# Optimization experiments

Measured on AMD Instinct MI355X. Metric: run time of the kernel, lower is better.

The kernel has to match this reference:

```python
import jax, jax.numpy as jnp
import numpy as np

B, S, D = 16, 1024, 1024
H = 8
QK = D // 8            # qk_dim = dim / qk_dim_div(8) = 128
EXP = D * 2            # expand_dim = dim * expand_factor(2) = 2048
V = D                  # v_dim = dim
RESIDUAL_DEPTH = 384   # hyp['net']['residual_depth'] (init scale only)
NUM_BLOCKS = 8         # hyp['net']['num_blocks'] (init scale only)
NEG = -1e30            # stand-in for -inf in the masked positions


def setup_inputs() -> dict:
    key = jax.random.key(0)
    k0, k1, k2 = jax.random.split(key, 3)
    x = jax.random.normal(k0, (B, S, D), jnp.float32)
    norm_w = jnp.ones((D,), jnp.float32)  # LayerNorm weight (bias=False)
    expand_w = (0.5 / RESIDUAL_DEPTH**0.5 / 2.0) * jax.random.normal(
        k1, (2 * QK + 2 * EXP, D), jnp.float32)
    project_w = (1.0 / RESIDUAL_DEPTH**0.5 / 2.0 / NUM_BLOCKS) * jax.random.normal(
        k2, (D, EXP), jnp.float32)
    pos_bias_mult = jnp.array(1.0, jnp.float32)
    return {
        "x": x,
        "norm_w": norm_w,
        "expand_w": expand_w,
        "project_w": project_w,
        "pos_bias_mult": pos_bias_mult,
        "first_acting_token_idx": 512,
        "last_acting_token_idx": 768,
    }


def _make_mask(pos_bias_mult, seq_len, first_idx, last_idx, dtype):
    idx = jnp.arange(seq_len)
    rel = (idx[None, :] - idx[:, None]).astype(dtype)   # j - i  (ALiBi-like)
    causal = idx[None, :] <= idx[:, None]               # tril incl. diagonal
    bias = jax.nn.softplus(pos_bias_mult) * rel
    mask = jnp.where(causal, bias, NEG)
    if first_idx is not None:
        assert last_idx is not None and last_idx > first_idx
        # torch: idx >= seq_len -> None -> slice from 0
        fi = 0 if first_idx >= seq_len else first_idx
        li = 0 if last_idx >= seq_len else last_idx
        override = (idx[:, None] >= fi) & (idx[None, :] >= li)
        mask = jnp.where(override, bias, mask)
    return mask


def reference(x, norm_w, expand_w, project_w, pos_bias_mult,
              first_acting_token_idx, last_acting_token_idx):
    Bx, Sx, Dx = x.shape
    residual = x
    mask = _make_mask(pos_bias_mult, Sx, first_acting_token_idx,
                      last_acting_token_idx, x.dtype)  # [S, S]

    # LayerNorm (bias-free)
    mu = x.mean(-1, keepdims=True)
    xc = x - mu
    var = (xc * xc).mean(-1, keepdims=True)
    xn = xc * jax.lax.rsqrt(var + 1e-5) * norm_w

    # fused expand projection, then split q / k / linear / pre_gelu
    proj = jnp.einsum('bsd,ed->bse', xn, expand_w)
    q = proj[..., :QK]
    k = proj[..., QK:2 * QK]
    lin = proj[..., 2 * QK:2 * QK + EXP]
    pre = proj[..., 2 * QK + EXP:]
    geglu = lin * jax.nn.gelu(pre, approximate=False)

    # linear_value = False: both local and attention-value come from geglu
    geglu_local = geglu[..., :EXP - V]   # [B, S, EXP-V]
    geglu_value = geglu[..., EXP - V:]   # [B, S, V]

    dh_q = QK // H
    dh_v = V // H
    qh = q.reshape(Bx, Sx, H, dh_q).transpose(0, 2, 1, 3)
    kh = k.reshape(Bx, Sx, H, dh_q).transpose(0, 2, 1, 3)
    vh = geglu_value.reshape(Bx, Sx, H, dh_v).transpose(0, 2, 1, 3)

    scale = 1.0 / np.sqrt(dh_q)  # SDPA default: 1/sqrt(E), E = query head dim
    scores = jnp.einsum('bhqd,bhkd->bhqk', qh, kh) * scale + mask
    attn = jax.nn.softmax(scores, axis=-1)
    outh = jnp.einsum('bhqk,bhkd->bhqd', attn, vh)
    attention = outh.transpose(0, 2, 1, 3).reshape(Bx, Sx, V)
    # NOTE: geglu_local's head rearrange + inverse rearrange is an identity.

    out = jnp.einsum('bse,de->bsd',
                     jnp.concatenate([geglu_local, attention], axis=-1),
                     project_w)
    return residual + out
```

## Files before the change

kernel.cpp:

```cpp
#include <hip/hip_runtime.h>
#include <hip/hip_bf16.h>
#include <cstdint>
#include <cstddef>

#define S_LEN   1024
#define D_DIM   1024
#define QK_DIM  128
#define EXP_DIM 2048
#define H_HEADS 8
#define DH_Q    16
#define DH_V    128
#define M_ROWS  16384

typedef __bf16 bf16;
typedef __bf16 b16x4 __attribute__((ext_vector_type(4)));
typedef __bf16 b16x8 __attribute__((ext_vector_type(8)));
typedef float  fx4   __attribute__((ext_vector_type(4)));
typedef float  f32x16 __attribute__((ext_vector_type(16)));

__device__ __forceinline__ void load_lds16(const bf16* g, bf16* l) {
    __builtin_amdgcn_global_load_lds(
        (const __attribute__((address_space(1))) void*)g,
        (__attribute__((address_space(3))) void*)l, 16, 0, 0);
}

__global__ __launch_bounds__(256) void convert_kernel(const float* __restrict__ src,
                                                      bf16* __restrict__ dst, int n4) {
    const int i = blockIdx.x * 256 + threadIdx.x;
    if (i >= n4) return;
    const fx4 v = ((const fx4*)src)[i];
    b16x4 o;
#pragma unroll
    for (int k = 0; k < 4; ++k) o[k] = (bf16)v[k];
    ((b16x4*)dst)[i] = o;
}

__global__ __launch_bounds__(256) void convert_expand_kernel(const float* __restrict__ src,
                                                             bf16* __restrict__ dst) {
    const int i = blockIdx.x * 256 + threadIdx.x;
    const int orow = i >> 8, col = i & 255;
    int irow;
    if (orow < 256) {
        irow = orow;
    } else {
        const int t = orow - 256;
        const int c = t >> 5, j = t & 31;
        irow = (j < 16) ? (256 + c * 16 + j) : (2304 + c * 16 + (j - 16));
    }
    const fx4 v = ((const fx4*)src)[irow * 256 + col];
    b16x4 o;
#pragma unroll
    for (int k = 0; k < 4; ++k) o[k] = (bf16)v[k];
    ((b16x4*)dst)[i] = o;
}

__global__ __launch_bounds__(256) void ln_kernel(const float* __restrict__ x,
                                                 const float* __restrict__ w,
                                                 bf16* __restrict__ xn) {
    const int row = blockIdx.x;
    const int tid = threadIdx.x;
    const fx4 t = ((const fx4*)x)[(size_t)row * 256 + tid];
    float v[4];
    float s = 0.f, ss = 0.f;
#pragma unroll
    for (int i = 0; i < 4; ++i) { v[i] = t[i]; s += v[i]; ss += v[i] * v[i]; }
#pragma unroll
    for (int off = 32; off >= 1; off >>= 1) {
        s  += __shfl_xor(s,  off);
        ss += __shfl_xor(ss, off);
    }
    __shared__ float ls[4], lss[4];
    const int wave = tid >> 6;
    if ((tid & 63) == 0) { ls[wave] = s; lss[wave] = ss; }
    __syncthreads();
    s  = ls[0]  + ls[1]  + ls[2]  + ls[3];
    ss = lss[0] + lss[1] + lss[2] + lss[3];
    const float mu  = s * (1.f / D_DIM);
    const float var = ss * (1.f / D_DIM) - mu * mu;
    const float r   = rsqrtf(var + 1e-5f);
    const fx4 w4 = ((const fx4*)w)[tid];
    b16x4 o4;
#pragma unroll
    for (int i = 0; i < 4; ++i) o4[i] = (bf16)((v[i] - mu) * r * w4[i]);
    ((b16x4*)(xn + (size_t)row * D_DIM))[tid] = o4;
}

__device__ __forceinline__ float gelu_exact(float x) {
    return 0.5f * x * (1.f + erff(x * 0.70710678118654752f));
}

__device__ __forceinline__ void tile_map(int& tm, int& tn) {
    const int NT = gridDim.x, MT = gridDim.y;
    const int lin = blockIdx.y * NT + blockIdx.x;
    if ((MT & 31) == 0 && (NT & 3) == 0) {
        const int xcd = lin & 7, slot = lin >> 3;
        const int MB  = MT >> 3;
        const int cnc = NT >> 2;
        const int c = slot >> 4, w = slot & 15;
        const int cm = c / cnc, cn = c - cm * cnc;
        tm = xcd * MB + cm * 4 + (w >> 2);
        tn = cn * 4 + (w & 3);
    } else { tm = blockIdx.y; tn = blockIdx.x; }
}

__device__ __forceinline__ void tile_map256(int& tm, int& tn) {
    const int NT = gridDim.x, MT = gridDim.y;
    const int lin = blockIdx.y * NT + blockIdx.x;
    if ((MT & 31) == 0 && (NT & 3) == 0) {
        const int xcd = lin & 7, slot = lin >> 3;
        const int MB  = MT >> 3;
        const int cnc = NT >> 2;
        const int c = slot >> 4, w = slot & 15;
        const int cm = c / cnc, cn = c - cm * cnc;
        tm = xcd * MB + cm * 4 + (w >> 2);
        tn = cn * 4 + (w & 3);
    } else { tm = blockIdx.y; tn = blockIdx.x; }
}

template <int EPI>
__global__ __launch_bounds__(256) void gemm_bt(const bf16* __restrict__ A,
                                               const bf16* __restrict__ W,
                                               const float* __restrict__ R,
                                               bf16* __restrict__ C,
                                               bf16* __restrict__ VH,
                                               float* __restrict__ OutF,
                                               int M, int N, int K) {
    __shared__ bf16 As[128 * 32];
    __shared__ bf16 Ws[128 * 32];
    const int tid  = threadIdx.x;
    const int wave = tid >> 6, lane = tid & 63;
    int tmi, tni;
    tile_map(tmi, tni);
    const int tile_n = tni * 128;
    const int tile_m = tmi * 128;
    const int m_off = (wave >> 1) * 64, n_off = (wave & 1) * 64;

    fx4 acc[4][4] = {};

    const int c0 = wave * 128 + lane;
    const int c1 = c0 + 64;
    const int r0 = c0 >> 2, cc0 = (c0 & 3) * 8;
    const int r1 = c1 >> 2, cc1 = (c1 & 3) * 8;

    const int mrow = lane & 15, quad = lane >> 4;

    for (int k0 = 0; k0 < K; k0 += 32) {
        load_lds16(A + (size_t)(tile_m + r0) * K + k0 + cc0, &As[c0 * 8]);
        load_lds16(A + (size_t)(tile_m + r1) * K + k0 + cc1, &As[c1 * 8]);
        load_lds16(W + (size_t)(tile_n + r0) * K + k0 + cc0, &Ws[c0 * 8]);
        load_lds16(W + (size_t)(tile_n + r1) * K + k0 + cc1, &Ws[c1 * 8]);
        __syncthreads();

        b16x8 af[4], bfr[4];
#pragma unroll
        for (int i = 0; i < 4; ++i) {
            af[i]  = *(const b16x8*)&As[(m_off + i * 16 + mrow) * 32 + quad * 8];
            bfr[i] = *(const b16x8*)&Ws[(n_off + i * 16 + mrow) * 32 + quad * 8];
        }
#pragma unroll
        for (int mi = 0; mi < 4; ++mi)
#pragma unroll
            for (int ni = 0; ni < 4; ++ni)
                acc[mi][ni] = __builtin_amdgcn_mfma_f32_16x16x32_bf16(
                    af[mi], bfr[ni], acc[mi][ni], 0, 0, 0);
        __syncthreads();
    }

    const int lcol = lane & 15, lrow4 = (lane >> 4) * 4;
#pragma unroll
    for (int mi = 0; mi < 4; ++mi)
#pragma unroll
        for (int ni = 0; ni < 4; ++ni)
#pragma unroll
            for (int r = 0; r < 4; ++r) {
                const int gr = tile_m + m_off + mi * 16 + lrow4 + r;
                const int gc = tile_n + n_off + ni * 16 + lcol;
                const float a = acc[mi][ni][r];
                if (EPI == 0) {
                    C[(size_t)gr * N + gc] = (bf16)a;
                } else if (EPI == 1) {
                    const size_t idx = (size_t)gr * N + gc;
                    OutF[idx] = a + R[idx];
                }
            }
}

__device__ __forceinline__ b16x8 lds_frag_swz(const bf16* buf, int r, int colb) {
    const int p = (r << 7) + ((((colb >> 4) ^ r) & 7) << 4) + (colb & 15);
    return *(const b16x8*)((const char*)buf + p);
}

template <int EPI>
__global__ __launch_bounds__(512, 2) void gemm256(const bf16* __restrict__ A,
                                                  const bf16* __restrict__ W,
                                                  const float* __restrict__ R,
                                                  bf16* __restrict__ C,
                                                  bf16* __restrict__ VH,
                                                  float* __restrict__ OutF,
                                                  int M, int N, int K) {
    __shared__ bf16 Abuf[2][16384];
    __shared__ bf16 Bbuf[2][16384];
    const int tid  = threadIdx.x;
    const int wave = tid >> 6, lane = tid & 63;
    const int wm = wave >> 2, wn = wave & 3;
    const int l15 = lane & 15, quad = lane >> 4;

    int tmi, tni;
    tile_map256(tmi, tni);
    const int tile_m = tmi * 256, tile_n = tni * 256;

    const int srow = tid >> 3;
    const int scol = (((tid & 7) ^ ((tid >> 3) & 7))) * 8;
    size_t offA[4], offB[4];
#pragma unroll
    for (int s = 0; s < 4; ++s) {
        offA[s] = (size_t)(tile_m + s * 64 + srow) * K + scol;
        offB[s] = (size_t)(tile_n + s * 64 + srow) * K + scol;
    }
    const int ldst = tid * 16;

    fx4 acc[8][4] = {};

    const int ntk = K >> 6;
    {
        char* a0 = (char*)&Abuf[0][0] + ldst;
        char* b0 = (char*)&Bbuf[0][0] + ldst;
        load_lds16(A + offA[0], (bf16*)(a0));
        load_lds16(A + offA[2], (bf16*)(a0 + 16384));
        load_lds16(W + offB[0], (bf16*)(b0));
        load_lds16(W + offB[1], (bf16*)(b0 + 8192));
        load_lds16(W + offB[2], (bf16*)(b0 + 16384));
        load_lds16(W + offB[3], (bf16*)(b0 + 24576));
        load_lds16(A + offA[1], (bf16*)(a0 + 8192));
        load_lds16(A + offA[3], (bf16*)(a0 + 24576));
    }

    for (int t = 0; t < ntk; ++t) {
        const int nb = t & 1;
        const int kt1 = (t + 1) << 6;
        const bool pf = (t + 1 < ntk);
        const bf16* ab = &Abuf[nb][0];
        const bf16* bb = &Bbuf[nb][0];
        char* adst = (char*)&Abuf[nb ^ 1][0] + ldst;
        char* bdst = (char*)&Bbuf[nb ^ 1][0] + ldst;

        b16x8 af[4][2];
        b16x8 bfv[2][2];

        asm volatile("s_waitcnt vmcnt(2)" ::: "memory");
        __builtin_amdgcn_s_barrier();
        __builtin_amdgcn_sched_barrier(0);
#pragma unroll
        for (int mi = 0; mi < 4; ++mi)
#pragma unroll
            for (int kk = 0; kk < 2; ++kk)
                af[mi][kk] = lds_frag_swz(ab, wm * 128 + mi * 16 + l15, kk * 64 + quad * 16);
#pragma unroll
        for (int ni = 0; ni < 2; ++ni)
#pragma unroll
            for (int kk = 0; kk < 2; ++kk)
                bfv[ni][kk] = lds_frag_swz(bb, wn * 64 + ni * 16 + l15, kk * 64 + quad * 16);
        if (pf) {
            load_lds16(A + offA[0] + kt1, (bf16*)(adst));
            load_lds16(A + offA[2] + kt1, (bf16*)(adst + 16384));
        }
        __builtin_amdgcn_s_setprio(1);
#pragma unroll
        for (int mi = 0; mi < 4; ++mi)
#pragma unroll
            for (int ni = 0; ni < 2; ++ni)
#pragma unroll
                for (int kk = 0; kk < 2; ++kk)
                    acc[mi][ni] = __builtin_amdgcn_mfma_f32_16x16x32_bf16(
                        af[mi][kk], bfv[ni][kk], acc[mi][ni], 0, 0, 0);
        __builtin_amdgcn_s_setprio(0);

        __builtin_amdgcn_s_barrier();
        __builtin_amdgcn_sched_barrier(0);
#pragma unroll
        for (int ni = 0; ni < 2; ++ni)
#pragma unroll
            for (int kk = 0; kk < 2; ++kk)
                bfv[ni][kk] = lds_frag_swz(bb, wn * 64 + (ni + 2) * 16 + l15, kk * 64 + quad * 16);
        if (pf) {
            load_lds16(W + offB[0] + kt1, (bf16*)(bdst));
            load_lds16(W + offB[1] + kt1, (bf16*)(bdst + 8192));
            load_lds16(W + offB[2] + kt1, (bf16*)(bdst + 16384));
            load_lds16(W + offB[3] + kt1, (bf16*)(bdst + 24576));
        }
        __builtin_amdgcn_s_setprio(1);
#pragma unroll
        for (int mi = 0; mi < 4; ++mi)
#pragma unroll
            for (int ni = 0; ni < 2; ++ni)
#pragma unroll
                for (int kk = 0; kk < 2; ++kk)
                    acc[mi][ni + 2] = __builtin_amdgcn_mfma_f32_16x16x32_bf16(
                        af[mi][kk], bfv[ni][kk], acc[mi][ni + 2], 0, 0, 0);
        __builtin_amdgcn_s_setprio(0);

        if (pf) asm volatile("s_waitcnt vmcnt(6)" ::: "memory");
        else    asm volatile("s_waitcnt vmcnt(0)" ::: "memory");
        __builtin_amdgcn_s_barrier();
        __builtin_amdgcn_sched_barrier(0);
#pragma unroll
        for (int mi = 0; mi < 4; ++mi)
#pragma unroll
            for (int kk = 0; kk < 2; ++kk)
                af[mi][kk] = lds_frag_swz(ab, wm * 128 + (mi + 4) * 16 + l15, kk * 64 + quad * 16);
        if (pf) {
            load_lds16(A + offA[1] + kt1, (bf16*)(adst + 8192));
            load_lds16(A + offA[3] + kt1, (bf16*)(adst + 24576));
        }
        __builtin_amdgcn_s_setprio(1);
#pragma unroll
        for (int mi = 0; mi < 4; ++mi)
#pragma unroll
            for (int ni = 0; ni < 2; ++ni)
#pragma unroll
                for (int kk = 0; kk < 2; ++kk)
                    acc[mi + 4][ni + 2] = __builtin_amdgcn_mfma_f32_16x16x32_bf16(
                        af[mi][kk], bfv[ni][kk], acc[mi + 4][ni + 2], 0, 0, 0);
        __builtin_amdgcn_s_setprio(0);

        __builtin_amdgcn_s_barrier();
        __builtin_amdgcn_sched_barrier(0);
#pragma unroll
        for (int ni = 0; ni < 2; ++ni)
#pragma unroll
            for (int kk = 0; kk < 2; ++kk)
                bfv[ni][kk] = lds_frag_swz(bb, wn * 64 + ni * 16 + l15, kk * 64 + quad * 16);
        __builtin_amdgcn_s_setprio(1);
#pragma unroll
        for (int mi = 0; mi < 4; ++mi)
#pragma unroll
            for (int ni = 0; ni < 2; ++ni)
#pragma unroll
                for (int kk = 0; kk < 2; ++kk)
                    acc[mi + 4][ni] = __builtin_amdgcn_mfma_f32_16x16x32_bf16(
                        af[mi][kk], bfv[ni][kk], acc[mi + 4][ni], 0, 0, 0);
        __builtin_amdgcn_s_setprio(0);
        __builtin_amdgcn_s_barrier();
        __builtin_amdgcn_sched_barrier(0);
    }

    const int rbase = tile_m + wm * 128 + quad * 4;
    if (EPI == 2) {
        const int gb = ((tile_n + wn * 64) >> 1) + l15;
#pragma unroll
        for (int mi = 0; mi < 8; ++mi)
#pragma unroll
            for (int np = 0; np < 2; ++np) {
                const int gcol = gb + np * 16;
#pragma unroll
                for (int r = 0; r < 4; ++r) {
                    const int gr = rbase + mi * 16 + r;
                    const float l = acc[mi][2 * np][r];
                    const float p = acc[mi][2 * np + 1][r];
                    const float g = l * gelu_exact(p);
                    if (gcol < 1024) C[(size_t)gr * 2048 + gcol] = (bf16)g;
                    else             VH[(size_t)gr * 1024 + (gcol - 1024)] = (bf16)g;
                }
            }
    } else {
#pragma unroll
        for (int mi = 0; mi < 8; ++mi)
#pragma unroll
            for (int ni = 0; ni < 4; ++ni)
#pragma unroll
                for (int r = 0; r < 4; ++r) {
                    const int gr = rbase + mi * 16 + r;
                    const int gc = tile_n + wn * 64 + ni * 16 + l15;
                    const float a = acc[mi][ni][r];
                    if (EPI == 0) {
                        C[(size_t)gr * N + gc] = (bf16)a;
                    } else {
                        const size_t idx = (size_t)gr * N + gc;
                        OutF[idx] = a + R[idx];
                    }
                }
    }
}

__global__ __launch_bounds__(512) void attn_kernel(const bf16* __restrict__ qk,
                                                   const bf16* __restrict__ vh,
                                                   const float* __restrict__ pbmv,
                                                   const int* __restrict__ fip,
                                                   const int* __restrict__ lip,
                                                   bf16* __restrict__ concatb) {
    const int lin = blockIdx.y * gridDim.x + blockIdx.x;
    const int xcd = lin & 7, slot = lin >> 3;
    const int bh = xcd * 16 + (slot >> 3);
    const int qt = slot & 7;
    const int b = bh >> 3, h = bh & 7;
    const int q0 = qt * 128;
    const int tid  = threadIdx.x;
    const int wave = tid >> 6, lane = tid & 63;
    const int lm = lane & 31, lh = lane >> 5;
    const int qq = wave >> 1, sect = wave & 1;

    __shared__ float Ps[128][68];
    __shared__ bf16  Pb[128][72];
    __shared__ bf16  Vt[128][72];
    __shared__ float Mrow[128], Lrow[128], Arow[128];

    const float pm = pbmv[0];
    const float sp = (pm > 20.f) ? pm : log1pf(expf(pm));
    int fi = fip[0], li = lip[0];
    if (fi >= S_LEN) fi = 0;
    if (li >= S_LEN) li = 0;

    const b16x8 qfrag = *(const b16x8*)(qk
        + ((size_t)(b * S_LEN + q0 + qq * 32 + lm)) * 256 + h * DH_Q + lh * 8);

    f32x16 accO[2] = {};
    if (tid < 128) { Mrow[tid] = -3e38f; Lrow[tid] = 0.f; }

    const int vkey = tid & 63;
    const int vd   = (tid >> 6) * 16;
    const int srow = wave * 16 + (lane >> 2);
    const int skq  = (lane & 3) * 16;

    const int qmax = q0 + 127;
    for (int k0 = 0; k0 < S_LEN; k0 += 64) {
        const bool any = (k0 <= qmax) || ((qmax >= fi) && (k0 + 63 >= li));
        if (!any) continue;

        __syncthreads();

#pragma unroll
        for (int i = 0; i < 2; ++i) {
            const int d0 = vd + i * 8;
            const b16x8 v8 = *(const b16x8*)(vh
                + ((size_t)(b * S_LEN + k0 + vkey)) * D_DIM + h * DH_V + d0);
#pragma unroll
            for (int j = 0; j < 8; ++j) Vt[d0 + j][vkey] = v8[j];
        }

        {
            const b16x8 kfrag = *(const b16x8*)(qk
                + ((size_t)(b * S_LEN + k0 + sect * 32 + lm)) * 256
                + QK_DIM + h * DH_Q + lh * 8);
            f32x16 z = {};
            const f32x16 S = __builtin_amdgcn_mfma_f32_32x32x16_bf16(qfrag, kfrag, z, 0, 0, 0);
#pragma unroll
            for (int r = 0; r < 16; ++r) {
                const int row = qq * 32 + (r & 3) + 8 * (r >> 2) + 4 * lh;
                Ps[row][sect * 32 + lm] = S[r];
            }
        }
        __syncthreads();

        {
            const int rg = q0 + srow;
            float s[16];
#pragma unroll
            for (int i = 0; i < 4; ++i) {
                const fx4 t = *(const fx4*)&Ps[srow][skq + i * 4];
#pragma unroll
                for (int j = 0; j < 4; ++j) {
                    const int jg = k0 + skq + i * 4 + j;
                    const bool act = (jg <= rg) || ((rg >= fi) && (jg >= li));
                    s[i * 4 + j] = act ? (t[j] * 0.25f + sp * (float)(jg - rg)) : -3e38f;
                }
            }
            float mloc = -3e38f;
#pragma unroll
            for (int i = 0; i < 16; ++i) mloc = fmaxf(mloc, s[i]);
            mloc = fmaxf(mloc, __shfl_xor(mloc, 1));
            mloc = fmaxf(mloc, __shfl_xor(mloc, 2));
            const float m_old = Mrow[srow];
            const float m_new = fmaxf(m_old, mloc);
            const float alpha = (m_old <= -1e29f) ? 0.f : __expf(m_old - m_new);
            float lsum = 0.f;
            b16x8 p0, p1;
#pragma unroll
            for (int i = 0; i < 16; ++i) {
                const float p = (s[i] <= -1e29f) ? 0.f : __expf(s[i] - m_new);
                lsum += p;
                if (i < 8) p0[i] = (bf16)p; else p1[i - 8] = (bf16)p;
            }
            lsum += __shfl_xor(lsum, 1);
            lsum += __shfl_xor(lsum, 2);
            *(b16x8*)&Pb[srow][skq]     = p0;
            *(b16x8*)&Pb[srow][skq + 8] = p1;
            if ((lane & 3) == 0) {
                Mrow[srow] = m_new;
                Lrow[srow] = alpha * Lrow[srow] + lsum;
                Arow[srow] = alpha;
            }
        }
        __syncthreads();

        {
#pragma unroll
            for (int r = 0; r < 16; ++r) {
                const float al = Arow[qq * 32 + (r & 3) + 8 * (r >> 2) + 4 * lh];
                accO[0][r] *= al;
                accO[1][r] *= al;
            }
            b16x8 Af[4];
#pragma unroll
            for (int ks = 0; ks < 4; ++ks)
                Af[ks] = *(const b16x8*)&Pb[qq * 32 + lm][ks * 16 + lh * 8];
#pragma unroll
            for (int nb = 0; nb < 2; ++nb)
#pragma unroll
                for (int ks = 0; ks < 4; ++ks) {
                    const b16x8 Bf = *(const b16x8*)&Vt[sect * 64 + nb * 32 + lm][ks * 16 + lh * 8];
                    accO[nb] = __builtin_amdgcn_mfma_f32_32x32x16_bf16(Af[ks], Bf, accO[nb], 0, 0, 0);
                }
        }
    }

#pragma unroll
    for (int r = 0; r < 16; ++r) {
        const int row = qq * 32 + (r & 3) + 8 * (r >> 2) + 4 * lh;
        const float L = Lrow[row];
        const float inv = (L > 0.f) ? 1.f / L : 0.f;
        const size_t base = ((size_t)(b * S_LEN + q0 + row)) * EXP_DIM
                          + EXP_DIM / 2 + h * DH_V + sect * 64 + lm;
#pragma unroll
        for (int nb = 0; nb < 2; ++nb)
            concatb[base + nb * 32] = (bf16)(accO[nb][r] * inv);
    }
}

static constexpr size_t WS0_OFF = 0;
static constexpr size_t QK_OFF  = 67108864;
static constexpr size_t VH_OFF  = QK_OFF + 8388608;
static constexpr size_t EW_OFF  = VH_OFF + 33554432;
static constexpr size_t PW_OFF  = EW_OFF + 8912896;
static constexpr size_t WS_NEED = PW_OFF + 4194304;

extern "C" void kernel_launch(void* const* d_in, const int* in_sizes, int n_in,
                              void* d_out, int out_size, void* d_ws, size_t ws_size,
                              hipStream_t stream) {
    const float* x         = (const float*)d_in[0];
    const float* norm_w    = (const float*)d_in[1];
    const float* expand_w  = (const float*)d_in[2];
    const float* project_w = (const float*)d_in[3];
    const float* pbm       = (const float*)d_in[4];
    const int*   fip       = (const int*)d_in[5];
    const int*   lip       = (const int*)d_in[6];
    float* out = (float*)d_out;

    if (ws_size < WS_NEED) return;

    char* ws = (char*)d_ws;
    bf16* ws0 = (bf16*)(ws + WS0_OFF);
    bf16* qkb = (bf16*)(ws + QK_OFF);
    bf16* vh  = (bf16*)(ws + VH_OFF);
    bf16* ewb = (bf16*)(ws + EW_OFF);
    bf16* pwb = (bf16*)(ws + PW_OFF);
    bf16* xn  = (bf16*)d_out;

    convert_expand_kernel<<<4352, 256, 0, stream>>>(expand_w, ewb);
    convert_kernel<<<2048, 256, 0, stream>>>(project_w, pwb, 2097152 / 4);
    ln_kernel<<<M_ROWS, 256, 0, stream>>>(x, norm_w, xn);

    gemm_bt<0><<<dim3(2, M_ROWS / 128), 256, 0, stream>>>(
        xn, ewb, nullptr, qkb, nullptr, nullptr, M_ROWS, 256, D_DIM);
    gemm256<2><<<dim3(16, M_ROWS / 256), 512, 0, stream>>>(
        xn, ewb + (size_t)256 * D_DIM, nullptr, ws0, vh, nullptr, M_ROWS, 4096, D_DIM);
    attn_kernel<<<dim3(64, 16), 512, 0, stream>>>(qkb, vh, pbm, fip, lip, ws0);
    gemm256<1><<<dim3(4, M_ROWS / 256), 512, 0, stream>>>(
        ws0, pwb, x, nullptr, nullptr, out, M_ROWS, D_DIM, EXP_DIM);
}
```

Measured before the change: 505.4 us.

## Keep attention scores in registers via transposed MFMA and per-section row stats

Computes S^T with swapped MFMA operands so each lane holds one query row's scores, applying the mask, scale and bias and running the online softmax in registers instead of staging fp32 scores through LDS. Row max is combined across the two key sections through a small shared buffer, and running max/sum are kept per lane, with sums merged at the end. P fragments are assembled with cross-half shuffles and reused directly as MFMA A operands for the local half, cutting LDS traffic. This adds shuffle work and a small reduction sync, and it changes the softmax work split across lanes.

```diff
diff --git a/kernel.cpp b/kernel.cpp
--- a/kernel.cpp
+++ b/kernel.cpp
@@ -399,10 +399,11 @@
     const int lm = lane & 31, lh = lane >> 5;
     const int qq = wave >> 1, sect = wave & 1;
 
-    __shared__ float Ps[128][68];
     __shared__ bf16  Pb[128][72];
     __shared__ bf16  Vt[128][72];
-    __shared__ float Mrow[128], Lrow[128], Arow[128];
+    __shared__ float Msect[2][128];
+    __shared__ float Lsect[2][128];
+    __shared__ float Arow[128];
 
     const float pm = pbmv[0];
     const float sp = (pm > 20.f) ? pm : log1pf(expf(pm));
@@ -414,12 +415,12 @@
         + ((size_t)(b * S_LEN + q0 + qq * 32 + lm)) * 256 + h * DH_Q + lh * 8);
 
     f32x16 accO[2] = {};
-    if (tid < 128) { Mrow[tid] = -3e38f; Lrow[tid] = 0.f; }
+    float m_run = -3e38f, l_run = 0.f;
 
     const int vkey = tid & 63;
     const int vd   = (tid >> 6) * 16;
-    const int srow = wave * 16 + (lane >> 2);
-    const int skq  = (lane & 3) * 16;
+    const int myrow = qq * 32 + lm;
+    const int rg    = q0 + myrow;
 
     const int qmax = q0 + 127;
     for (int k0 = 0; k0 < S_LEN; k0 += 64) {
@@ -437,58 +438,62 @@
             for (int j = 0; j < 8; ++j) Vt[d0 + j][vkey] = v8[j];
         }
 
+        float s[16];
+        float mx = -3e38f;
         {
             const b16x8 kfrag = *(const b16x8*)(qk
                 + ((size_t)(b * S_LEN + k0 + sect * 32 + lm)) * 256
                 + QK_DIM + h * DH_Q + lh * 8);
             f32x16 z = {};
-            const f32x16 S = __builtin_amdgcn_mfma_f32_32x32x16_bf16(qfrag, kfrag, z, 0, 0, 0);
+            const f32x16 S = __builtin_amdgcn_mfma_f32_32x32x16_bf16(kfrag, qfrag, z, 0, 0, 0);
 #pragma unroll
             for (int r = 0; r < 16; ++r) {
-                const int row = qq * 32 + (r & 3) + 8 * (r >> 2) + 4 * lh;
-                Ps[row][sect * 32 + lm] = S[r];
+                const int jg = k0 + sect * 32 + (r & 3) + 8 * (r >> 2) + 4 * lh;
+                const bool act = (jg <= rg) || ((rg >= fi) && (jg >= li));
+                s[r] = act ? (S[r] * 0.25f + sp * (float)(jg - rg)) : -3e38f;
+                mx = fmaxf(mx, s[r]);
             }
         }
+        mx = fmaxf(mx, __shfl_xor(mx, 32));
+        if (lh == 0) Msect[sect][myrow] = mx;
         __syncthreads();
 
-        {
-            const int rg = q0 + srow;
-            float s[16];
-#pragma unroll
-            for (int i = 0; i < 4; ++i) {
-                const fx4 t = *(const fx4*)&Ps[srow][skq + i * 4];
-#pragma unroll
-                for (int j = 0; j < 4; ++j) {
-                    const int jg = k0 + skq + i * 4 + j;
-                    const bool act = (jg <= rg) || ((rg >= fi) && (jg >= li));
-                    s[i * 4 + j] = act ? (t[j] * 0.25f + sp * (float)(jg - rg)) : -3e38f;
-                }
+        const float m_tile = fmaxf(Msect[0][myrow], Msect[1][myrow]);
+        const float m_new  = fmaxf(m_run, m_tile);
+        const float alpha  = (m_run <= -1e29f) ? 0.f : __expf(m_run - m_new);
+        l_run *= alpha;
+        bf16 pbv[16];
+#pragma unroll
+        for (int r = 0; r < 16; ++r) {
+            const float p = (s[r] <= -1e29f) ? 0.f : __expf(s[r] - m_new);
+            l_run += p;
+            pbv[r] = (bf16)p;
+        }
+        m_run = m_new;
+        if (sect == 0 && lh == 0) Arow[myrow] = alpha;
+
+        uint32_t ou[8], pu[8];
+#pragma unroll
+        for (int i = 0; i < 8; ++i) {
+            union { bf16 hx[2]; uint32_t u; } c;
+            c.hx[0] = pbv[2 * i]; c.hx[1] = pbv[2 * i + 1];
+            ou[i] = c.u;
+        }
+#pragma unroll
+        for (int i = 0; i < 8; ++i) pu[i] = (uint32_t)__shfl_xor((int)ou[i], 32);
+        b16x8 pa[2];
+#pragma unroll
+        for (int ks = 0; ks < 2; ++ks) {
+            union { uint32_t u[4]; b16x8 v; } a;
+            if (lh == 0) {
+                a.u[0] = ou[4 * ks];     a.u[1] = ou[4 * ks + 1];
+                a.u[2] = pu[4 * ks];     a.u[3] = pu[4 * ks + 1];
+            } else {
+                a.u[0] = pu[4 * ks + 2]; a.u[1] = pu[4 * ks + 3];
+                a.u[2] = ou[4 * ks + 2]; a.u[3] = ou[4 * ks + 3];
             }
-            float mloc = -3e38f;
-#pragma unroll
-            for (int i = 0; i < 16; ++i) mloc = fmaxf(mloc, s[i]);
-            mloc = fmaxf(mloc, __shfl_xor(mloc, 1));
-            mloc = fmaxf(mloc, __shfl_xor(mloc, 2));
-            const float m_old = Mrow[srow];
-            const float m_new = fmaxf(m_old, mloc);
-            const float alpha = (m_old <= -1e29f) ? 0.f : __expf(m_old - m_new);
-            float lsum = 0.f;
-            b16x8 p0, p1;
-#pragma unroll
-            for (int i = 0; i < 16; ++i) {
-                const float p = (s[i] <= -1e29f) ? 0.f : __expf(s[i] - m_new);
-                lsum += p;
-                if (i < 8) p0[i] = (bf16)p; else p1[i - 8] = (bf16)p;
-            }
-            lsum += __shfl_xor(lsum, 1);
-            lsum += __shfl_xor(lsum, 2);
-            *(b16x8*)&Pb[srow][skq]     = p0;
-            *(b16x8*)&Pb[srow][skq + 8] = p1;
-            if ((lane & 3) == 0) {
-                Mrow[srow] = m_new;
-                Lrow[srow] = alpha * Lrow[srow] + lsum;
-                Arow[srow] = alpha;
-            }
+            pa[ks] = a.v;
+            *(b16x8*)&Pb[myrow][sect * 32 + ks * 16 + lh * 8] = pa[ks];
         }
         __syncthreads();
 
@@ -500,9 +505,17 @@
                 accO[1][r] *= al;
             }
             b16x8 Af[4];
-#pragma unroll
-            for (int ks = 0; ks < 4; ++ks)
-                Af[ks] = *(const b16x8*)&Pb[qq * 32 + lm][ks * 16 + lh * 8];
+            if (sect == 0) {
+                Af[0] = pa[0];
+                Af[1] = pa[1];
+                Af[2] = *(const b16x8*)&Pb[qq * 32 + lm][2 * 16 + lh * 8];
+                Af[3] = *(const b16x8*)&Pb[qq * 32 + lm][3 * 16 + lh * 8];
+            } else {
+                Af[0] = *(const b16x8*)&Pb[qq * 32 + lm][0 * 16 + lh * 8];
+                Af[1] = *(const b16x8*)&Pb[qq * 32 + lm][1 * 16 + lh * 8];
+                Af[2] = pa[0];
+                Af[3] = pa[1];
+            }
 #pragma unroll
             for (int nb = 0; nb < 2; ++nb)
 #pragma unroll
@@ -513,10 +526,16 @@
         }
     }
 
+    {
+        const float lt = l_run + __shfl_xor(l_run, 32);
+        if (lh == 0) Lsect[sect][myrow] = lt;
+    }
+    __syncthreads();
+
 #pragma unroll
     for (int r = 0; r < 16; ++r) {
         const int row = qq * 32 + (r & 3) + 8 * (r >> 2) + 4 * lh;
-        const float L = Lrow[row];
+        const float L = Lsect[0][row] + Lsect[1][row];
         const float inv = (L > 0.f) ? 1.f / L : 0.f;
         const size_t base = ((size_t)(b * S_LEN + q0 + row)) * EXP_DIM
                           + EXP_DIM / 2 + h * DH_V + sect * 64 + lm;
```

After: 496.1 us. About the same (-1.8%).
